# Kernel tuning notes

Measured on AMD Instinct MI355X. Metric: run time of the kernel, lower is better.

Reference implementation:

```python
import jax, jax.numpy as jnp
import numpy as np

B, S, C, T, WU = 32, 8, 16, 64, 16   # batch, scatterers, candidates, time, warm-up
LSTM, FC = 128, 256                  # lstm_units, fc_units
CONCAT = WU * LSTM + (T - WU) * FC   # 14336


def setup_inputs() -> dict:
    key = jax.random.key(0)
    ks = jax.random.split(key, 16)
    w = lambda k, shape, s=0.05: (jax.random.normal(k, shape, jnp.float32) * s)
    return {
        "inputs": jax.random.normal(ks[0], (B, S, C, T, 2), jnp.float32),
        "Wi": w(ks[1], (2, 4 * LSTM)),
        "Wh": w(ks[2], (LSTM, 4 * LSTM)),
        "b_lstm": jnp.zeros((4 * LSTM,), jnp.float32),
        "Wp": w(ks[3], (LSTM, 2)),
        "bp": jnp.zeros((2,), jnp.float32),
        "W1": w(ks[4], (2, FC)),
        "b1": jnp.zeros((FC,), jnp.float32),
        "W2": w(ks[5], (FC, FC)),
        "b2": jnp.zeros((FC,), jnp.float32),
        "Wc": w(ks[6], (CONCAT, FC), 0.01),
        "bc": jnp.zeros((FC,), jnp.float32),
        "Wprob": w(ks[7], (FC, 2)),
        "bprob": jnp.zeros((2,), jnp.float32),
        "Wasso": w(ks[8], (FC, 1)),
        "basso": jnp.zeros((1,), jnp.float32),
        "warm_up_length": WU,
    }


def reference(inputs, Wi, Wh, b_lstm, Wp, bp, W1, b1, W2, b2,
              Wc, bc, Wprob, bprob, Wasso, basso, warm_up_length):
    Bb, Ss, Cc, Tt, _ = inputs.shape
    N = Bb * Ss * Cc
    Wl = int(warm_up_length)
    Tr = Tt - Wl
    U = Wh.shape[0]
    Fc = W2.shape[1]
    x = inputs.reshape(N, Tt, 2)

    def cell(carry, xt):  # Keras LSTMCell step
        h, c = carry
        z = xt @ Wi + h @ Wh + b_lstm            # [N, 4U]
        i, f, g, o = jnp.split(z, 4, axis=-1)
        c = jax.nn.sigmoid(f) * c + jax.nn.sigmoid(i) * jnp.tanh(g)
        h = jax.nn.sigmoid(o) * jnp.tanh(c)
        return (h, c), h

    h0 = jnp.zeros((N, U), inputs.dtype)
    c0 = jnp.zeros((N, U), inputs.dtype)
    # warm-up: teacher-forced steps over the first Wl frames
    (h, c), hs = jax.lax.scan(cell, (h0, c0), jnp.swapaxes(x[:, :Wl], 0, 1))
    pred = jnp.tanh(h @ Wp + bp)                  # dense_lstm_pred on last warm-up output

    def ar(carry, _):
        p, h, c = carry
        (h, c), hn = cell((h, c), p)
        p2 = jnp.tanh(hn @ Wp + bp)
        return (p2, h, c), p2

    _, preds = jax.lax.scan(ar, (pred, h, c), None, length=Tr)
    preds = jnp.swapaxes(preds, 0, 1)             # [N, Tr, 2]

    # association heads (dropout = identity at inference)
    t1 = jnp.tanh(preds @ W1 + b1)                # [N, Tr, FC]
    t2 = jnp.tanh(t1 @ W2 + b2)                   # [N, Tr, FC]
    flat_lstm = jnp.swapaxes(hs, 0, 1).reshape(N, Wl * U)
    concat = jnp.concatenate([flat_lstm, t2.reshape(N, Tr * Fc)], axis=-1)
    ev = jnp.tanh(concat @ Wc + bc)               # [N, FC]
    prob = jax.nn.softmax(ev @ Wprob + bprob, axis=-1)
    cost = ev @ Wasso + basso                     # [N, 1]

    out = jnp.zeros((4, Bb, Ss, Cc, Tr, 2), inputs.dtype)
    out = out.at[0].set(preds.reshape(Bb, Ss, Cc, Tr, 2))
    out = out.at[1, :, :, :, 0, 0].set(cost.reshape(Bb, Ss, Cc))
    out = out.at[2, :, :, :, 0].set(prob.reshape(Bb, Ss, Cc, 2))
    out = out.at[3].set(inputs[:, :, :, Wl:, :])
    return out
```

## Files before the change

### kernel.cpp

```cpp
#include <hip/hip_runtime.h>
#include <stdint.h>

typedef float  f32x4  __attribute__((ext_vector_type(4)));
typedef short  short8 __attribute__((ext_vector_type(8)));

#define DEV __device__ __forceinline__

#define L2E  1.4426950408889634f
#define L2E2 2.8853900817779268f

DEV float ex2(float x){ float r; asm("v_exp_f32 %0, %1" : "=v"(r) : "v"(x)); return r; }
DEV unsigned cvtpk_bf16(float lo, float hi){
  unsigned r; asm("v_cvt_pk_bf16_f32 %0, %1, %2" : "=v"(r) : "v"(lo), "v"(hi)); return r;
}

DEV unsigned short f2bf(float x){
  union { float f; unsigned u; } v; v.f = x;
  unsigned r = v.u + 0x7fffu + ((v.u >> 16) & 1u);
  return (unsigned short)(r >> 16);
}
DEV float bf2f(unsigned short u){
  union { unsigned u; float f; } v; v.u = ((unsigned)u) << 16;
  return v.f;
}
DEV float tanhx_(float x){ return 1.f - 2.f*__builtin_amdgcn_rcpf(1.f + ex2(x*L2E2)); }
DEV float sig_ps(float z){ return __builtin_amdgcn_rcpf(1.f + ex2(z)); }
DEV float tanh_ps(float z){ return 1.f - 2.f*__builtin_amdgcn_rcpf(1.f + ex2(z)); }

template<bool SWZ, bool GSCALE>
__global__ void __launch_bounds__(256) transpose_bf16_k(const float* __restrict__ src,
    unsigned short* __restrict__ dst, int R, int C)
{
  __shared__ float tile[32][33];
  const int tx = threadIdx.x & 31, ty = threadIdx.x >> 5;
  const int c0 = blockIdx.x * 32, r0 = blockIdx.y * 32;
  #pragma unroll
  for (int m = 0; m < 4; ++m){
    int r = ty + m*8;
    tile[r][tx] = src[(size_t)(r0 + r) * C + (c0 + tx)];
  }
  __syncthreads();
  #pragma unroll
  for (int m = 0; m < 4; ++m){
    int cc = c0 + ty + m*8;
    int k  = r0 + tx;
    int k2 = SWZ ? (k ^ ((cc & 7) << 3)) : k;
    float v = tile[tx][ty + m*8];
    if (GSCALE) v *= ((cc >> 7) == 2) ? L2E2 : -L2E;
    dst[(size_t)cc * R + k2] = f2bf(v);
  }
}

__global__ void __launch_bounds__(256) copy_out3_k(const float* __restrict__ in,
                                                   float* __restrict__ out3)
{
  int i = blockIdx.x * 256 + threadIdx.x;
  int n = i / 24, q = i - n*24;
  f32x4 v = *(const f32x4*)(in + (size_t)n*128 + 32 + q*4);
  *(f32x4*)(out3 + (size_t)n*96 + q*4) = v;
}

__global__ void __launch_bounds__(512, 2) lstm_k(
    const float* __restrict__ inputs, const float* __restrict__ Wi,
    const unsigned short* __restrict__ WhT, const float* __restrict__ bl,
    const float* __restrict__ Wp, const float* __restrict__ bp,
    unsigned short* __restrict__ concat, float* __restrict__ out0)
{
  __shared__ __align__(16) unsigned char hbuf[2*16*16*16];
  __shared__ __align__(16) unsigned char hwu[16*16*256];
  __shared__ float predb[48][16][2];
  __shared__ float xwu[16][33];
  const int tid = threadIdx.x, lane = tid & 63, w = tid >> 6;
  const int n0 = blockIdx.x * 16;
  const int col = lane & 15;
  const int u = w*16 + col;
  const int rbase = (lane >> 4) * 4;

  { int s = tid >> 5, e = tid & 31;
    xwu[s][e] = inputs[(size_t)(n0 + s)*128 + e]; }

  short8 bfrag[4][4];
  #pragma unroll
  for (int g = 0; g < 4; ++g){
    const unsigned short* p = WhT + (size_t)(g*128 + u) * 128;
    #pragma unroll
    for (int kt = 0; kt < 4; ++kt)
      bfrag[g][kt] = *(const short8*)(p + kt*32 + (lane >> 4)*8);
  }
  short8 wpf[4];
  #pragma unroll
  for (int kt = 0; kt < 4; ++kt){
    short8 v;
    #pragma unroll
    for (int j = 0; j < 8; ++j){
      int k = kt*32 + (lane >> 4)*8 + j;
      v[j] = (short)f2bf(Wp[k*2 + (col & 1)]);
    }
    wpf[kt] = v;
  }
  float wi0[4], wi1[4];
  f32x4 bbv[4];
  #pragma unroll
  for (int g = 0; g < 4; ++g){
    int c = g*128 + u;
    float sc = (g == 2) ? L2E2 : -L2E;
    wi0[g] = Wi[c] * sc; wi1[g] = Wi[512 + c] * sc;
    float b = bl[c] * sc;
    bbv[g] = (f32x4){b, b, b, b};
  }
  const float bpv = bp[col & 1];
  const f32x4 bpvv = (f32x4){bpv, bpv, bpv, bpv};
  float cst[4] = {0.f, 0.f, 0.f, 0.f};
  __syncthreads();

  #pragma unroll 1
  for (int t = 0; t < 64; ++t){
    const unsigned char* rd = hbuf + ((t + 1) & 1) * 4096;
    unsigned char*       wr = hbuf + (t & 1) * 4096;
    short8 afr[4];
    if (t > 0){
      #pragma unroll
      for (int kt = 0; kt < 4; ++kt)
        afr[kt] = *(const short8*)(rd + (kt*4 + (lane >> 4))*256 + col*16);
    }
    float x0[4], x1[4];
    if (t < 16){
      #pragma unroll
      for (int i = 0; i < 4; ++i){
        x0[i] = xwu[rbase + i][t*2]; x1[i] = xwu[rbase + i][t*2 + 1];
      }
    } else {
      f32x4 pacc = __builtin_amdgcn_mfma_f32_16x16x32_bf16(afr[0], wpf[0], bpvv, 0, 0, 0);
      pacc = __builtin_amdgcn_mfma_f32_16x16x32_bf16(afr[1], wpf[1], pacc, 0, 0, 0);
      pacc = __builtin_amdgcn_mfma_f32_16x16x32_bf16(afr[2], wpf[2], pacc, 0, 0, 0);
      pacc = __builtin_amdgcn_mfma_f32_16x16x32_bf16(afr[3], wpf[3], pacc, 0, 0, 0);
      float val[4];
      #pragma unroll
      for (int i = 0; i < 4; ++i) val[i] = tanhx_(pacc[i]);
      #pragma unroll
      for (int i = 0; i < 4; ++i){
        float ov_ = __shfl_xor(val[i], 1);
        x0[i] = (col & 1) ? ov_ : val[i];
        x1[i] = (col & 1) ? val[i] : ov_;
      }
      if (w == 0 && col < 2 && t >= 17){
        #pragma unroll
        for (int i = 0; i < 4; ++i) predb[t - 17][rbase + i][col] = val[i];
      }
    }
    f32x4 acc[4];
    if (t > 0){
      #pragma unroll
      for (int g = 0; g < 4; ++g)
        acc[g] = __builtin_amdgcn_mfma_f32_16x16x32_bf16(afr[0], bfrag[g][0], bbv[g], 0, 0, 0);
      #pragma unroll
      for (int kt = 1; kt < 4; ++kt){
        #pragma unroll
        for (int g = 0; g < 4; ++g)
          acc[g] = __builtin_amdgcn_mfma_f32_16x16x32_bf16(afr[kt], bfrag[g][kt], acc[g], 0, 0, 0);
      }
    } else {
      #pragma unroll
      for (int g = 0; g < 4; ++g) acc[g] = bbv[g];
    }
    float hf[4];
    #pragma unroll
    for (int i = 0; i < 4; ++i){
      float z0 = acc[0][i] + x0[i]*wi0[0] + x1[i]*wi1[0];
      float z1 = acc[1][i] + x0[i]*wi0[1] + x1[i]*wi1[1];
      float z2 = acc[2][i] + x0[i]*wi0[2] + x1[i]*wi1[2];
      float z3 = acc[3][i] + x0[i]*wi0[3] + x1[i]*wi1[3];
      float iv = sig_ps(z0), fv = sig_ps(z1), gv = tanh_ps(z2), ov = sig_ps(z3);
      float c = fv*cst[i] + iv*gv;
      cst[i] = c;
      hf[i] = ov * tanhx_(c);
    }
    unsigned p01 = cvtpk_bf16(hf[0], hf[1]);
    unsigned p23 = cvtpk_bf16(hf[2], hf[3]);
    unsigned short hb[4] = {
      (unsigned short)(p01 & 0xffffu), (unsigned short)(p01 >> 16),
      (unsigned short)(p23 & 0xffffu), (unsigned short)(p23 >> 16) };
    #pragma unroll
    for (int i = 0; i < 4; ++i){
      int r = rbase + i;
      *(unsigned short*)(wr + (u >> 3)*256 + r*16 + (u & 7)*2) = hb[i];
      if (t < 16)
        *(unsigned short*)(hwu + t*4096 + r*256 + u*2) = hb[i];
    }
    __syncthreads();
  }
  {
    const unsigned char* rd = hbuf + 4096;
    short8 afr[4];
    #pragma unroll
    for (int kt = 0; kt < 4; ++kt)
      afr[kt] = *(const short8*)(rd + (kt*4 + (lane >> 4))*256 + col*16);
    f32x4 pacc = __builtin_amdgcn_mfma_f32_16x16x32_bf16(afr[0], wpf[0], bpvv, 0, 0, 0);
    pacc = __builtin_amdgcn_mfma_f32_16x16x32_bf16(afr[1], wpf[1], pacc, 0, 0, 0);
    pacc = __builtin_amdgcn_mfma_f32_16x16x32_bf16(afr[2], wpf[2], pacc, 0, 0, 0);
    pacc = __builtin_amdgcn_mfma_f32_16x16x32_bf16(afr[3], wpf[3], pacc, 0, 0, 0);
    if (w == 0 && col < 2){
      #pragma unroll
      for (int i = 0; i < 4; ++i) predb[47][rbase + i][col] = tanhx_(pacc[i]);
    }
  }
  __syncthreads();
  for (int idx = tid; idx < 4096; idx += 512){
    int t = idx >> 8, s = (idx >> 4) & 15, j = idx & 15;
    short8 v = *(const short8*)(hwu + t*4096 + s*256 + j*16);
    *(short8*)((unsigned char*)concat + (size_t)(n0 + s)*28672
        + ((unsigned)(t*256 + j*16) ^ ((s & 7) << 4))) = v;
  }
  for (int idx = tid; idx < 1536; idx += 512){
    int s = idx / 96, r = idx - s*96;
    out0[(size_t)(n0 + s)*96 + r] = predb[r >> 1][s][r & 1];
  }
}

__global__ void __launch_bounds__(256) t1t2_k(
    const float* __restrict__ preds, const float* __restrict__ W1,
    const float* __restrict__ b1, const unsigned short* __restrict__ W2T,
    const float* __restrict__ b2, unsigned short* __restrict__ concat)
{
  __shared__ __align__(16) unsigned char t1buf[16*512];
  const int tid = threadIdx.x, lane = tid & 63, w = tid >> 6;

  short8 bfrag[4][8];
  {
    const int krow = (lane >> 4) * 8;
    #pragma unroll
    for (int nt = 0; nt < 4; ++nt){
      const unsigned short* p = W2T + (size_t)(w*64 + nt*16 + (lane & 15)) * 256;
      #pragma unroll
      for (int kt = 0; kt < 8; ++kt){
        bfrag[nt][kt] = *(const short8*)(p + kt*32 + krow);
      }
    }
  }
  float b2c[4];
  #pragma unroll
  for (int nt = 0; nt < 4; ++nt) b2c[nt] = b2[w*64 + nt*16 + (lane & 15)];
  float w1a[16], w1b[16], b1c[16];
  {
    const int k0 = (tid & 15) * 16;
    #pragma unroll
    for (int j = 0; j < 16; ++j){
      w1a[j] = W1[k0 + j]; w1b[j] = W1[256 + k0 + j]; b1c[j] = b1[k0 + j];
    }
  }
  const int lr = tid >> 4, k0 = (tid & 15) * 16;

  #pragma unroll 1
  for (int rt = 0; rt < 8; ++rt){
    const int r0 = blockIdx.x * 128 + rt * 16;
    {
      const float p0 = preds[(size_t)(r0 + lr)*2 + 0];
      const float p1 = preds[(size_t)(r0 + lr)*2 + 1];
      const int sw = (lr & 7) << 4;
      #pragma unroll
      for (int h = 0; h < 2; ++h){
        short8 t1v;
        #pragma unroll
        for (int j = 0; j < 8; ++j){
          int jj = h*8 + j;
          t1v[j] = (short)f2bf(tanhx_(p0*w1a[jj] + p1*w1b[jj] + b1c[jj]));
        }
        *(short8*)(t1buf + ((lr*512 + (k0 + h*8)*2) ^ sw)) = t1v;
      }
    }
    __syncthreads();
    f32x4 acc[4];
    #pragma unroll
    for (int nt = 0; nt < 4; ++nt) acc[nt] = (f32x4){0.f,0.f,0.f,0.f};
    {
      const int row = lane & 15;
      const int sw = (row & 7) << 4;
      #pragma unroll
      for (int kt = 0; kt < 8; ++kt){
        short8 a = *(const short8*)(t1buf + ((row*512 + (kt*32 + (lane>>4)*8)*2) ^ sw));
        #pragma unroll
        for (int nt = 0; nt < 4; ++nt){
          acc[nt] = __builtin_amdgcn_mfma_f32_16x16x32_bf16(a, bfrag[nt][kt], acc[nt], 0, 0, 0);
        }
      }
    }
    #pragma unroll
    for (int nt = 0; nt < 4; ++nt){
      const int col = w*64 + nt*16 + (lane & 15);
      #pragma unroll
      for (int i = 0; i < 4; ++i){
        int m = r0 + (lane >> 4)*4 + i;
        int n = m / 48, tt = m - n*48;
        unsigned short val = f2bf(tanhx_(acc[nt][i] + b2c[nt]));
        *(unsigned short*)((unsigned char*)concat + (size_t)n*28672
            + ((unsigned)((2048 + tt*256 + col)*2) ^ ((n & 7) << 4))) = val;
      }
    }
    __syncthreads();
  }
}

__global__ void __launch_bounds__(512, 2) ev_k(
    const unsigned short* __restrict__ concat, const unsigned short* __restrict__ WcT,
    float* __restrict__ partials)
{
  __shared__ __align__(16) unsigned char Abuf[128*128];
  __shared__ __align__(16) unsigned char Bbuf[256*128];
  const int tid = threadIdx.x, lane = tid & 63, w = tid >> 6;
  const int wm = w >> 2, wn = w & 3;
  const int n0 = blockIdx.x * 128;
  const int kbase = blockIdx.y * 1792;

  f32x4 acc[4][4];
  #pragma unroll
  for (int mt = 0; mt < 4; ++mt)
    #pragma unroll
    for (int nt = 0; nt < 4; ++nt) acc[mt][nt] = (f32x4){0.f,0.f,0.f,0.f};

  const int aoff = tid * 32;
  const int arow = aoff >> 7;
  const unsigned char* asrc = (const unsigned char*)concat + (size_t)(n0 + arow)*28672 + (aoff & 127);
  const int bcol = tid >> 1, bhalf = (tid & 1) * 64;
  const unsigned char* bsrc = (const unsigned char*)WcT + (size_t)bcol*28672 + bhalf;

  short8 ar0 = *(const short8*)(asrc + kbase*2);
  short8 ar1 = *(const short8*)(asrc + kbase*2 + 16);
  short8 br[4];
  #pragma unroll
  for (int kb = 0; kb < 4; ++kb) br[kb] = *(const short8*)(bsrc + kbase*2 + kb*16);

  #pragma unroll 1
  for (int ch = 0; ch < 28; ++ch){
    __syncthreads();
    *(short8*)(Abuf + aoff)      = ar0;
    *(short8*)(Abuf + aoff + 16) = ar1;
    #pragma unroll
    for (int kb = 0; kb < 4; ++kb) *(short8*)(Bbuf + bcol*128 + bhalf + kb*16) = br[kb];
    __syncthreads();
    if (ch < 27){
      const int kk2 = (kbase + (ch + 1)*64) * 2;
      ar0 = *(const short8*)(asrc + kk2);
      ar1 = *(const short8*)(asrc + kk2 + 16);
      #pragma unroll
      for (int kb = 0; kb < 4; ++kb) br[kb] = *(const short8*)(bsrc + kk2 + kb*16);
    }
    #pragma unroll
    for (int kt = 0; kt < 2; ++kt){
      const int kby = kt*64 + (lane >> 4)*16;
      short8 afr[4], bfr[4];
      #pragma unroll
      for (int mt = 0; mt < 4; ++mt){
        int row = wm*64 + mt*16 + (lane & 15);
        afr[mt] = *(const short8*)(Abuf + ((row*128 + kby) ^ ((row & 7) << 4)));
      }
      #pragma unroll
      for (int nt = 0; nt < 4; ++nt){
        int col = wn*64 + nt*16 + (lane & 15);
        bfr[nt] = *(const short8*)(Bbuf + ((col*128 + kby) ^ ((col & 7) << 4)));
      }
      #pragma unroll
      for (int mt = 0; mt < 4; ++mt)
        #pragma unroll
        for (int nt = 0; nt < 4; ++nt)
          acc[mt][nt] = __builtin_amdgcn_mfma_f32_16x16x32_bf16(afr[mt], bfr[nt], acc[mt][nt], 0, 0, 0);
    }
  }
  float* dst = partials + (size_t)blockIdx.y * (4096*256);
  #pragma unroll
  for (int mt = 0; mt < 4; ++mt){
    #pragma unroll
    for (int nt = 0; nt < 4; ++nt){
      #pragma unroll
      for (int i = 0; i < 4; ++i){
        int n = n0 + wm*64 + mt*16 + (lane >> 4)*4 + i;
        int col = wn*64 + nt*16 + (lane & 15);
        dst[(size_t)n*256 + col] = acc[mt][nt][i];
      }
    }
  }
}

__global__ void __launch_bounds__(256) heads_k(
    const float* __restrict__ partials, const float* __restrict__ bc,
    const float* __restrict__ Wprob, const float* __restrict__ bprob,
    const float* __restrict__ Wasso, const float* __restrict__ basso,
    float* __restrict__ out1, float* __restrict__ out2)
{
  __shared__ float evs[16][257];
  const int tid = threadIdx.x;
  const int nl = tid >> 4, part = tid & 15;
  const int n = blockIdx.x * 16 + nl;
  #pragma unroll
  for (int q = 0; q < 4; ++q){
    const int c = part*16 + q*4;
    f32x4 s = {0.f,0.f,0.f,0.f};
    #pragma unroll
    for (int p = 0; p < 8; ++p){
      s += *(const f32x4*)(partials + (size_t)p*1048576 + (size_t)n*256 + c);
    }
    #pragma unroll
    for (int j = 0; j < 4; ++j) evs[nl][c + j] = tanhx_(s[j] + bc[c + j]);
  }
  __syncthreads();
  float s0 = 0.f, s1 = 0.f, s2 = 0.f;
  #pragma unroll
  for (int j = 0; j < 16; ++j){
    int c = part*16 + j;
    float e = evs[nl][c];
    s0 += e * Wprob[c*2];
    s1 += e * Wprob[c*2 + 1];
    s2 += e * Wasso[c];
  }
  s0 += __shfl_xor(s0, 1); s1 += __shfl_xor(s1, 1); s2 += __shfl_xor(s2, 1);
  s0 += __shfl_xor(s0, 2); s1 += __shfl_xor(s1, 2); s2 += __shfl_xor(s2, 2);
  s0 += __shfl_xor(s0, 4); s1 += __shfl_xor(s1, 4); s2 += __shfl_xor(s2, 4);
  s0 += __shfl_xor(s0, 8); s1 += __shfl_xor(s1, 8); s2 += __shfl_xor(s2, 8);
  if (part == 0){
    float a0 = s0 + bprob[0], a1 = s1 + bprob[1];
    float m = fmaxf(a0, a1);
    float e0 = ex2((a0 - m)*L2E), e1 = ex2((a1 - m)*L2E);
    float inv = __builtin_amdgcn_rcpf(e0 + e1);
    out2[(size_t)n*96 + 0] = e0 * inv;
    out2[(size_t)n*96 + 1] = e1 * inv;
    out1[(size_t)n*96 + 0] = s2 + basso[0];
  }
}

extern "C" void kernel_launch(void* const* d_in, const int* in_sizes, int n_in,
                              void* d_out, int out_size, void* d_ws, size_t ws_size,
                              hipStream_t stream)
{
  (void)in_sizes; (void)n_in; (void)ws_size;
  const float* inputs = (const float*)d_in[0];
  const float* Wi     = (const float*)d_in[1];
  const float* Wh     = (const float*)d_in[2];
  const float* bl     = (const float*)d_in[3];
  const float* Wp     = (const float*)d_in[4];
  const float* bp     = (const float*)d_in[5];
  const float* W1     = (const float*)d_in[6];
  const float* b1     = (const float*)d_in[7];
  const float* W2     = (const float*)d_in[8];
  const float* b2     = (const float*)d_in[9];
  const float* Wc     = (const float*)d_in[10];
  const float* bc     = (const float*)d_in[11];
  const float* Wprob  = (const float*)d_in[12];
  const float* bprob  = (const float*)d_in[13];
  const float* Wasso  = (const float*)d_in[14];
  const float* basso  = (const float*)d_in[15];
  float* out = (float*)d_out;

  char* ws = (char*)d_ws;
  unsigned short* concat = (unsigned short*)ws;
  unsigned short* WhT    = (unsigned short*)(ws + 117440512);
  unsigned short* W2T    = (unsigned short*)(ws + 117571584);
  unsigned short* WcT    = (unsigned short*)(ws + 117702656);
  float*          parts  = (float*)(ws + 125042688);

  hipMemsetAsync(d_out, 0, (size_t)out_size * sizeof(float), stream);
  dim3 blk(256);
  transpose_bf16_k<false, true ><<<dim3(16, 4),  blk, 0, stream>>>(Wh, WhT, 128, 512);
  transpose_bf16_k<false, false><<<dim3(8, 8),   blk, 0, stream>>>(W2, W2T, 256, 256);
  transpose_bf16_k<true,  false><<<dim3(8, 448), blk, 0, stream>>>(Wc, WcT, 14336, 256);
  copy_out3_k<<<384, blk, 0, stream>>>(inputs, out + 3*393216);
  lstm_k<<<256, dim3(512), 0, stream>>>(inputs, Wi, WhT, bl, Wp, bp, concat, out);
  t1t2_k<<<1536, blk, 0, stream>>>(out, W1, b1, W2T, b2, concat);
  ev_k<<<dim3(32, 8), dim3(512), 0, stream>>>(concat, WcT, parts);
  heads_k<<<256, blk, 0, stream>>>(parts, bc, Wprob, bprob, Wasso, basso,
                                   out + 393216, out + 2*393216);
}
```

Baseline: 230.5 us.

## Fuse t1/t2 head computation with FC-part of Wc GEMM, skip concat roundtrip

```diff
diff --git a/kernel.cpp b/kernel.cpp
--- a/kernel.cpp
+++ b/kernel.cpp
@@ -18,10 +18,6 @@
   union { float f; unsigned u; } v; v.f = x;
   unsigned r = v.u + 0x7fffu + ((v.u >> 16) & 1u);
   return (unsigned short)(r >> 16);
-}
-DEV float bf2f(unsigned short u){
-  union { unsigned u; float f; } v; v.u = ((unsigned)u) << 16;
-  return v.f;
 }
 DEV float tanhx_(float x){ return 1.f - 2.f*__builtin_amdgcn_rcpf(1.f + ex2(x*L2E2)); }
 DEV float sig_ps(float z){ return __builtin_amdgcn_rcpf(1.f + ex2(z)); }
@@ -217,90 +213,122 @@
   }
 }
 
-__global__ void __launch_bounds__(256) t1t2_k(
+__global__ void __launch_bounds__(512, 2) t2ev_k(
     const float* __restrict__ preds, const float* __restrict__ W1,
     const float* __restrict__ b1, const unsigned short* __restrict__ W2T,
-    const float* __restrict__ b2, unsigned short* __restrict__ concat)
-{
-  __shared__ __align__(16) unsigned char t1buf[16*512];
+    const float* __restrict__ b2, const unsigned short* __restrict__ WcT2,
+    float* __restrict__ partials)
+{
+  __shared__ __align__(16) unsigned char t1buf[64*512];
+  __shared__ __align__(16) unsigned char t2buf[64*512];
   const int tid = threadIdx.x, lane = tid & 63, w = tid >> 6;
-
-  short8 bfrag[4][8];
-  {
-    const int krow = (lane >> 4) * 8;
-    #pragma unroll
-    for (int nt = 0; nt < 4; ++nt){
-      const unsigned short* p = W2T + (size_t)(w*64 + nt*16 + (lane & 15)) * 256;
-      #pragma unroll
-      for (int kt = 0; kt < 8; ++kt){
-        bfrag[nt][kt] = *(const short8*)(p + kt*32 + krow);
-      }
-    }
-  }
-  float b2c[4];
-  #pragma unroll
-  for (int nt = 0; nt < 4; ++nt) b2c[nt] = b2[w*64 + nt*16 + (lane & 15)];
+  const int n0 = blockIdx.x * 64;
+  const int tg = blockIdx.y;
+  const int lr = tid >> 4, k0 = (tid & 15) * 16;
+
   float w1a[16], w1b[16], b1c[16];
-  {
-    const int k0 = (tid & 15) * 16;
-    #pragma unroll
-    for (int j = 0; j < 16; ++j){
-      w1a[j] = W1[k0 + j]; w1b[j] = W1[256 + k0 + j]; b1c[j] = b1[k0 + j];
-    }
-  }
-  const int lr = tid >> 4, k0 = (tid & 15) * 16;
+  #pragma unroll
+  for (int j = 0; j < 16; ++j){
+    w1a[j] = W1[k0 + j]; w1b[j] = W1[256 + k0 + j]; b1c[j] = b1[k0 + j];
+  }
+  short8 bfrag[2][8];
+  float b2c[2];
+  #pragma unroll
+  for (int c2 = 0; c2 < 2; ++c2){
+    int col = w*32 + c2*16 + (lane & 15);
+    const unsigned short* p = W2T + (size_t)col * 256;
+    #pragma unroll
+    for (int kt = 0; kt < 8; ++kt)
+      bfrag[c2][kt] = *(const short8*)(p + kt*32 + (lane >> 4)*8);
+    b2c[c2] = b2[col];
+  }
+  f32x4 aev[4][2];
+  #pragma unroll
+  for (int rt = 0; rt < 4; ++rt){
+    aev[rt][0] = (f32x4){0.f,0.f,0.f,0.f};
+    aev[rt][1] = (f32x4){0.f,0.f,0.f,0.f};
+  }
 
   #pragma unroll 1
-  for (int rt = 0; rt < 8; ++rt){
-    const int r0 = blockIdx.x * 128 + rt * 16;
-    {
-      const float p0 = preds[(size_t)(r0 + lr)*2 + 0];
-      const float p1 = preds[(size_t)(r0 + lr)*2 + 1];
-      const int sw = (lr & 7) << 4;
-      #pragma unroll
-      for (int h = 0; h < 2; ++h){
+  for (int tl = 0; tl < 12; ++tl){
+    const int t = tg*12 + tl;
+    #pragma unroll
+    for (int h = 0; h < 2; ++h){
+      const int row = lr + h*32;
+      const float p0 = preds[(size_t)(n0 + row)*96 + t*2 + 0];
+      const float p1 = preds[(size_t)(n0 + row)*96 + t*2 + 1];
+      const int sw = (row & 7) << 4;
+      #pragma unroll
+      for (int hh = 0; hh < 2; ++hh){
         short8 t1v;
         #pragma unroll
         for (int j = 0; j < 8; ++j){
-          int jj = h*8 + j;
+          int jj = hh*8 + j;
           t1v[j] = (short)f2bf(tanhx_(p0*w1a[jj] + p1*w1b[jj] + b1c[jj]));
         }
-        *(short8*)(t1buf + ((lr*512 + (k0 + h*8)*2) ^ sw)) = t1v;
+        *(short8*)(t1buf + ((row*512 + (k0 + hh*8)*2) ^ sw)) = t1v;
       }
     }
     __syncthreads();
-    f32x4 acc[4];
-    #pragma unroll
-    for (int nt = 0; nt < 4; ++nt) acc[nt] = (f32x4){0.f,0.f,0.f,0.f};
-    {
-      const int row = lane & 15;
+    #pragma unroll
+    for (int rt = 0; rt < 4; ++rt){
+      f32x4 acc[2] = {(f32x4){0.f,0.f,0.f,0.f}, (f32x4){0.f,0.f,0.f,0.f}};
+      const int row = rt*16 + (lane & 15);
       const int sw = (row & 7) << 4;
       #pragma unroll
       for (int kt = 0; kt < 8; ++kt){
         short8 a = *(const short8*)(t1buf + ((row*512 + (kt*32 + (lane>>4)*8)*2) ^ sw));
+        acc[0] = __builtin_amdgcn_mfma_f32_16x16x32_bf16(a, bfrag[0][kt], acc[0], 0, 0, 0);
+        acc[1] = __builtin_amdgcn_mfma_f32_16x16x32_bf16(a, bfrag[1][kt], acc[1], 0, 0, 0);
+      }
+      #pragma unroll
+      for (int c2 = 0; c2 < 2; ++c2){
+        const int col = w*32 + c2*16 + (lane & 15);
         #pragma unroll
-        for (int nt = 0; nt < 4; ++nt){
-          acc[nt] = __builtin_amdgcn_mfma_f32_16x16x32_bf16(a, bfrag[nt][kt], acc[nt], 0, 0, 0);
+        for (int i = 0; i < 4; ++i){
+          int rw = rt*16 + (lane >> 4)*4 + i;
+          unsigned short val = f2bf(tanhx_(acc[c2][i] + b2c[c2]));
+          *(unsigned short*)(t2buf + ((unsigned)(rw*512 + col*2) ^ ((rw & 7) << 4))) = val;
         }
       }
     }
-    #pragma unroll
-    for (int nt = 0; nt < 4; ++nt){
-      const int col = w*64 + nt*16 + (lane & 15);
+    __syncthreads();
+    #pragma unroll
+    for (int c2 = 0; c2 < 2; ++c2){
+      const int col = w*32 + c2*16 + (lane & 15);
+      const unsigned short* bp = WcT2 + (size_t)col*12288 + t*256 + (lane >> 4)*8;
+      short8 bW[8];
+      #pragma unroll
+      for (int kt = 0; kt < 8; ++kt) bW[kt] = *(const short8*)(bp + kt*32);
+      #pragma unroll
+      for (int rt = 0; rt < 4; ++rt){
+        const int row = rt*16 + (lane & 15);
+        const int sw = (row & 7) << 4;
+        #pragma unroll
+        for (int kt = 0; kt < 8; ++kt){
+          short8 a = *(const short8*)(t2buf + ((row*512 + (kt*32 + (lane>>4)*8)*2) ^ sw));
+          aev[rt][c2] = __builtin_amdgcn_mfma_f32_16x16x32_bf16(a, bW[kt], aev[rt][c2], 0, 0, 0);
+        }
+      }
+    }
+    __syncthreads();
+  }
+  float* dst = partials + (size_t)tg * 1048576;
+  #pragma unroll
+  for (int rt = 0; rt < 4; ++rt){
+    #pragma unroll
+    for (int c2 = 0; c2 < 2; ++c2){
       #pragma unroll
       for (int i = 0; i < 4; ++i){
-        int m = r0 + (lane >> 4)*4 + i;
-        int n = m / 48, tt = m - n*48;
-        unsigned short val = f2bf(tanhx_(acc[nt][i] + b2c[nt]));
-        *(unsigned short*)((unsigned char*)concat + (size_t)n*28672
-            + ((unsigned)((2048 + tt*256 + col)*2) ^ ((n & 7) << 4))) = val;
-      }
-    }
-    __syncthreads();
-  }
-}
-
-__global__ void __launch_bounds__(512, 2) ev_k(
+        int n = n0 + rt*16 + (lane >> 4)*4 + i;
+        int cc = w*32 + c2*16 + (lane & 15);
+        dst[(size_t)n*256 + cc] = aev[rt][c2][i];
+      }
+    }
+  }
+}
+
+__global__ void __launch_bounds__(512, 2) evl_k(
     const unsigned short* __restrict__ concat, const unsigned short* __restrict__ WcT,
     float* __restrict__ partials)
 {
@@ -309,7 +337,7 @@
   const int tid = threadIdx.x, lane = tid & 63, w = tid >> 6;
   const int wm = w >> 2, wn = w & 3;
   const int n0 = blockIdx.x * 128;
-  const int kbase = blockIdx.y * 1792;
+  const int kbase = blockIdx.y * 1024;
 
   f32x4 acc[4][4];
   #pragma unroll
@@ -330,14 +358,14 @@
   for (int kb = 0; kb < 4; ++kb) br[kb] = *(const short8*)(bsrc + kbase*2 + kb*16);
 
   #pragma unroll 1
-  for (int ch = 0; ch < 28; ++ch){
+  for (int ch = 0; ch < 16; ++ch){
     __syncthreads();
     *(short8*)(Abuf + aoff)      = ar0;
     *(short8*)(Abuf + aoff + 16) = ar1;
     #pragma unroll
     for (int kb = 0; kb < 4; ++kb) *(short8*)(Bbuf + bcol*128 + bhalf + kb*16) = br[kb];
     __syncthreads();
-    if (ch < 27){
+    if (ch < 15){
       const int kk2 = (kbase + (ch + 1)*64) * 2;
       ar0 = *(const short8*)(asrc + kk2);
       ar1 = *(const short8*)(asrc + kk2 + 16);
@@ -374,7 +402,7 @@
       for (int i = 0; i < 4; ++i){
         int n = n0 + wm*64 + mt*16 + (lane >> 4)*4 + i;
         int col = wn*64 + nt*16 + (lane & 15);
-        dst[(size_t)n*256 + col] = acc[mt][nt][i];
+        dst[(size_t)n*256 + col] += acc[mt][nt][i];
       }
     }
   }
@@ -395,7 +423,7 @@
     const int c = part*16 + q*4;
     f32x4 s = {0.f,0.f,0.f,0.f};
     #pragma unroll
-    for (int p = 0; p < 8; ++p){
+    for (int p = 0; p < 4; ++p){
       s += *(const f32x4*)(partials + (size_t)p*1048576 + (size_t)n*256 + c);
     }
     #pragma unroll
@@ -454,17 +482,19 @@
   unsigned short* WhT    = (unsigned short*)(ws + 117440512);
   unsigned short* W2T    = (unsigned short*)(ws + 117571584);
   unsigned short* WcT    = (unsigned short*)(ws + 117702656);
-  float*          parts  = (float*)(ws + 125042688);
+  unsigned short* WcT2   = (unsigned short*)(ws + 125042688);
+  float*          parts  = (float*)(ws + 131334144);
 
   hipMemsetAsync(d_out, 0, (size_t)out_size * sizeof(float), stream);
   dim3 blk(256);
   transpose_bf16_k<false, true ><<<dim3(16, 4),  blk, 0, stream>>>(Wh, WhT, 128, 512);
   transpose_bf16_k<false, false><<<dim3(8, 8),   blk, 0, stream>>>(W2, W2T, 256, 256);
   transpose_bf16_k<true,  false><<<dim3(8, 448), blk, 0, stream>>>(Wc, WcT, 14336, 256);
+  transpose_bf16_k<false, false><<<dim3(8, 384), blk, 0, stream>>>(Wc + 2048*256, WcT2, 12288, 256);
   copy_out3_k<<<384, blk, 0, stream>>>(inputs, out + 3*393216);
   lstm_k<<<256, dim3(512), 0, stream>>>(inputs, Wi, WhT, bl, Wp, bp, concat, out);
-  t1t2_k<<<1536, blk, 0, stream>>>(out, W1, b1, W2T, b2, concat);
-  ev_k<<<dim3(32, 8), dim3(512), 0, stream>>>(concat, WcT, parts);
+  t2ev_k<<<dim3(64, 4), dim3(512), 0, stream>>>(out, W1, b1, W2T, b2, WcT2, parts);
+  evl_k<<<dim3(32, 2), dim3(512), 0, stream>>>(concat, WcT, parts);
   heads_k<<<256, blk, 0, stream>>>(parts, bc, Wprob, bprob, Wasso, basso,
                                    out + 393216, out + 2*393216);
 }
```

Measured after the change: 250.8 us. 1.09x slower.
